# Optimization experiments

Hardware: AMD Instinct MI355X
Metric: run time of the kernel (lower is better)

## Reference

```python
import jax, jax.numpy as jnp
import numpy as np

H, W = 2000, 1000  # T_out buffer: (1, 2000, 1000); conv spatial grid matches
FILL = -9999.0


def _winit(k, o, c):
    return jax.random.normal(k, (o, c), jnp.float32) * (1.0 / np.sqrt(c))


def setup_inputs() -> dict:
    key = jax.random.key(0)
    ks = jax.random.split(key, 6)
    inp = jax.random.normal(ks[0], (1, 9, H, W), dtype=jnp.float32)
    T_out = jnp.zeros((1, H, W), dtype=jnp.float32)
    flat = jnp.arange(H * W, dtype=jnp.int32)
    T_indices = jnp.stack([flat // W, flat % W]).reshape(2, H, W)
    return {
        "input": inp,
        "T_out": T_out,
        "T_indices": T_indices,
        "w1": _winit(ks[1], 18, 9), "b1": jnp.zeros((18,), jnp.float32),
        "w2": _winit(ks[2], 36, 18), "b2": jnp.zeros((36,), jnp.float32),
        "w3": _winit(ks[3], 36, 36), "b3": jnp.zeros((36,), jnp.float32),
        "w4": _winit(ks[4], 1, 36), "b4": jnp.zeros((1,), jnp.float32),
    }


def _conv1x1(x, w, b):
    # 1x1 conv == channel matmul: x (b,c,h,w), w (o,c)
    return jnp.einsum('bchw,oc->bohw', x, w) + b[None, :, None, None]


def reference(input, T_out, T_indices, w1, b1, w2, b2, w3, b3, w4, b4):
    x = jax.nn.relu(_conv1x1(input, w1, b1))
    x = jax.nn.relu(_conv1x1(x, w2, b2))
    x = jax.nn.relu(_conv1x1(x, w3, b3))
    x = _conv1x1(x, w4, b4)  # (1,1,H,W)
    # fill buffer with -9999 then indexed scatter of the fused scores
    T = jnp.full(T_out.shape, FILL, dtype=T_out.dtype)
    T = T.at[:, T_indices[0], T_indices[1]].set(x[0, 0])
    # MaxPool2d([1,1000]) -> max over W; MaxPool2d([2000,1]) -> max over H
    out1 = T.max(axis=2).squeeze()  # (2000,)
    out2 = T.max(axis=1).squeeze()  # (1000,)
    return (out1, out2)
```

## Files before the change

kernel.cpp:

```cpp
#include <hip/hip_runtime.h>

typedef _Float16 f16x8 __attribute__((ext_vector_type(8)));
typedef _Float16 f16x4 __attribute__((ext_vector_type(4)));
typedef __fp16 h16x2 __attribute__((ext_vector_type(2)));
typedef float f32x4 __attribute__((ext_vector_type(4)));

#define HH 2000
#define WW 1000
#define HWSZ (HH * WW)
#define NEG_INF (-3.0e38f)

__device__ __forceinline__ unsigned fenc(float f) {
    unsigned u = __float_as_uint(f);
    return (u & 0x80000000u) ? ~u : (u | 0x80000000u);
}
__device__ __forceinline__ float fdec(unsigned k) {
    unsigned u = (k & 0x80000000u) ? (k & 0x7fffffffu) : ~k;
    return __uint_as_float(u);
}

__global__ void decode_buckets(unsigned* __restrict__ buck, int n) {
    int i = blockIdx.x * blockDim.x + threadIdx.x;
    if (i < n) {
        unsigned k = buck[i];
        ((float*)buck)[i] = fdec(k);
    }
}


__global__ __launch_bounds__(128) void mlp_max_mfma(
    const float* __restrict__ in,
    const float* __restrict__ w1, const float* __restrict__ b1,
    const float* __restrict__ w2, const float* __restrict__ b2,
    const float* __restrict__ w3, const float* __restrict__ b3,
    const float* __restrict__ w4, const float* __restrict__ b4,
    unsigned* __restrict__ rowbuck, unsigned* __restrict__ colbuck) {
    __shared__ _Float16 albuf[2][2 * 1280];
    __shared__ float rowsm[2][16][16];

    const int tx = threadIdx.x;
    const int wv = threadIdx.y;
    const int px = tx & 15;
    const int q = tx >> 4;

    _Float16* s0buf1 = &albuf[wv][0];
    _Float16* s0buf2 = &albuf[wv][640];
    _Float16* s1buf1 = &albuf[wv][1280];
    _Float16* s1buf2 = &albuf[wv][1920];

    if (q == 0) {
        const f16x4 binit = {(_Float16)1.f, (_Float16)0.f, (_Float16)0.f, (_Float16)0.f};
        *(f16x4*)&s0buf2[px * 40 + 36] = binit;
        *(f16x4*)&s1buf2[px * 40 + 36] = binit;
    }

    f16x8 A1[2], A2[3], A3s0[3], A3s1[3];
#pragma unroll
    for (int t = 0; t < 2; ++t) {
        const int m = t * 16 + px;
#pragma unroll
        for (int j = 0; j < 8; ++j) {
            float v = 0.f;
            if (m < 18) {
                if (j == 0) v = w1[m * 9 + q];
                else if (j == 1) v = w1[m * 9 + 4 + q];
                else if (j == 2) {
                    if (q == 0) v = w1[m * 9 + 8];
                    else if (q == 1) v = b1[m];
                }
            }
            A1[t][j] = (_Float16)v;
        }
    }
#pragma unroll
    for (int t = 0; t < 3; ++t) {
        const int m = t * 16 + px;
#pragma unroll
        for (int j = 0; j < 8; ++j) {
            const int k = q * 8 + j;
            float v = 0.f;
            if (m < 36) {
                if (k < 18) v = w2[m * 18 + k];
                else if (k == 18) v = b2[m];
            }
            A2[t][j] = (_Float16)v;
        }
    }
#pragma unroll
    for (int t = 0; t < 3; ++t) {
        const int m = t * 16 + px;
#pragma unroll
        for (int j = 0; j < 8; ++j) {
            const int k = q * 8 + j;
            float v = 0.f;
            if (m < 36 && k < 32) v = w3[m * 36 + k];
            A3s0[t][j] = (_Float16)v;
            float v2 = 0.f;
            const int k2 = 32 + k;
            if (m < 36) {
                if (k2 < 36) v2 = w3[m * 36 + k2];
                else if (k2 == 36) v2 = b3[m];
            }
            A3s1[t][j] = (_Float16)v2;
        }
    }

    h16x2 w4p[3][2];
#pragma unroll
    for (int t = 0; t < 3; ++t)
#pragma unroll
        for (int i = 0; i < 2; ++i) {
            const int c0 = t * 16 + q * 4 + 2 * i;
            const int c1 = c0 + 1;
            w4p[t][i] = __builtin_amdgcn_cvt_pkrtz(c0 < 36 ? w4[c0] : 0.f,
                                                   c1 < 36 ? w4[c1] : 0.f);
        }
    const float b4s = b4[0];

    const int col = blockIdx.x * 32 + wv * 16 + px;
    const int colc = (col < WW) ? col : (WW - 1);
    const bool colok = (col < WW);
    const int rb = blockIdx.y * 16;

    float colmax = NEG_INF;
    const f32x4 zf4 = {0.f, 0.f, 0.f, 0.f};
    const h16x2 z2 = {(__fp16)0.f, (__fp16)0.f};

    union U8 { f16x8 v; h16x2 h[4]; };
    union U4 { f16x4 v; h16x2 h[2]; };

    const int off0 = q * HWSZ + colc;
    const int off1 = (4 + q) * HWSZ + colc;
    const int off2 = 8 * HWSZ + colc;
    const float j2fill = (q == 1) ? 1.f : 0.f;

    float ca[3], cb[3], na[3], nb[3];

    auto LOAD = [&](int r, float (&v0)[3], float (&v1)[3]) {
        const float* rbase = in + (size_t)r * WW;
        v0[0] = rbase[off0]; v1[0] = rbase[off0 + WW];
        v0[1] = rbase[off1]; v1[1] = rbase[off1 + WW];
        float x0 = j2fill, x1 = j2fill;
        if (q == 0) { x0 = rbase[off2]; x1 = rbase[off2 + WW]; }
        v0[2] = x0; v1[2] = x1;
    };

    auto COMPUTE = [&](int it, const float (&v0)[3], const float (&v1)[3]) {
        U8 b0u, b1u;
        b0u.h[0] = __builtin_amdgcn_cvt_pkrtz(v0[0], v0[1]);
        b0u.h[1] = __builtin_amdgcn_cvt_pkrtz(v0[2], 0.f);
        b0u.h[2] = z2; b0u.h[3] = z2;
        b1u.h[0] = __builtin_amdgcn_cvt_pkrtz(v1[0], v1[1]);
        b1u.h[1] = __builtin_amdgcn_cvt_pkrtz(v1[2], 0.f);
        b1u.h[2] = z2; b1u.h[3] = z2;
        const f16x8 bin0 = b0u.v;
        const f16x8 bin1 = b1u.v;

        f32x4 D1a[2], D1b[2];
#pragma unroll
        for (int t = 0; t < 2; ++t) {
            D1a[t] = __builtin_amdgcn_mfma_f32_16x16x32_f16(A1[t], bin0, zf4, 0, 0, 0);
            D1b[t] = __builtin_amdgcn_mfma_f32_16x16x32_f16(A1[t], bin1, zf4, 0, 0, 0);
        }
#pragma unroll
        for (int t = 0; t < 2; ++t) {
            U4 h0, h1;
            h0.h[0] = __builtin_elementwise_max(
                __builtin_amdgcn_cvt_pkrtz(D1a[t][0], D1a[t][1]), z2);
            h0.h[1] = __builtin_elementwise_max(
                __builtin_amdgcn_cvt_pkrtz(D1a[t][2], D1a[t][3]), z2);
            h1.h[0] = __builtin_elementwise_max(
                __builtin_amdgcn_cvt_pkrtz(D1b[t][0], D1b[t][1]), z2);
            h1.h[1] = __builtin_elementwise_max(
                __builtin_amdgcn_cvt_pkrtz(D1b[t][2], D1b[t][3]), z2);
            if (t == 1 && q == 0) {
                h0.v[2] = (_Float16)1.f;
                h1.v[2] = (_Float16)1.f;
            }
            *(f16x4*)&s0buf1[px * 40 + t * 16 + q * 4] = h0.v;
            *(f16x4*)&s1buf1[px * 40 + t * 16 + q * 4] = h1.v;
        }
        const f16x8 B2a = *(const f16x8*)&s0buf1[px * 40 + q * 8];
        const f16x8 B2b = *(const f16x8*)&s1buf1[px * 40 + q * 8];

        f32x4 D2a[3], D2b[3];
#pragma unroll
        for (int t = 0; t < 3; ++t) {
            D2a[t] = __builtin_amdgcn_mfma_f32_16x16x32_f16(A2[t], B2a, zf4, 0, 0, 0);
            D2b[t] = __builtin_amdgcn_mfma_f32_16x16x32_f16(A2[t], B2b, zf4, 0, 0, 0);
        }
#pragma unroll
        for (int t = 0; t < 3; ++t) {
            U4 h0, h1;
            h0.h[0] = __builtin_elementwise_max(
                __builtin_amdgcn_cvt_pkrtz(D2a[t][0], D2a[t][1]), z2);
            h0.h[1] = __builtin_elementwise_max(
                __builtin_amdgcn_cvt_pkrtz(D2a[t][2], D2a[t][3]), z2);
            h1.h[0] = __builtin_elementwise_max(
                __builtin_amdgcn_cvt_pkrtz(D2b[t][0], D2b[t][1]), z2);
            h1.h[1] = __builtin_elementwise_max(
                __builtin_amdgcn_cvt_pkrtz(D2b[t][2], D2b[t][3]), z2);
            if (t < 2) {
                *(f16x4*)&s0buf2[px * 40 + t * 16 + q * 4] = h0.v;
                *(f16x4*)&s1buf2[px * 40 + t * 16 + q * 4] = h1.v;
            } else if (q == 0) {
                *(f16x4*)&s0buf2[px * 40 + 32] = h0.v;
                *(f16x4*)&s1buf2[px * 40 + 32] = h1.v;
            }
        }
        const f16x8 B3a0 = *(const f16x8*)&s0buf2[px * 40 + q * 8];
        const f16x8 B3b0 = *(const f16x8*)&s1buf2[px * 40 + q * 8];
        const f16x8 B3a1 = *(const f16x8*)&s0buf2[px * 40 + 32];
        const f16x8 B3b1 = *(const f16x8*)&s1buf2[px * 40 + 32];

        f32x4 D3a[3], D3b[3];
#pragma unroll
        for (int t = 0; t < 3; ++t) {
            D3a[t] = __builtin_amdgcn_mfma_f32_16x16x32_f16(A3s0[t], B3a0, zf4, 0, 0, 0);
            D3a[t] = __builtin_amdgcn_mfma_f32_16x16x32_f16(A3s1[t], B3a1, D3a[t], 0, 0, 0);
            D3b[t] = __builtin_amdgcn_mfma_f32_16x16x32_f16(A3s0[t], B3b0, zf4, 0, 0, 0);
            D3b[t] = __builtin_amdgcn_mfma_f32_16x16x32_f16(A3s1[t], B3b1, D3b[t], 0, 0, 0);
        }

        float sa0 = 0.f, sa1 = 0.f, sb0 = 0.f, sb1 = 0.f;
#pragma unroll
        for (int t = 0; t < 3; ++t) {
            const h16x2 pa0 = __builtin_elementwise_max(
                __builtin_amdgcn_cvt_pkrtz(D3a[t][0], D3a[t][1]), z2);
            const h16x2 pa1 = __builtin_elementwise_max(
                __builtin_amdgcn_cvt_pkrtz(D3a[t][2], D3a[t][3]), z2);
            const h16x2 pb0 = __builtin_elementwise_max(
                __builtin_amdgcn_cvt_pkrtz(D3b[t][0], D3b[t][1]), z2);
            const h16x2 pb1 = __builtin_elementwise_max(
                __builtin_amdgcn_cvt_pkrtz(D3b[t][2], D3b[t][3]), z2);
            sa0 = __builtin_amdgcn_fdot2(pa0, w4p[t][0], sa0, false);
            sa1 = __builtin_amdgcn_fdot2(pa1, w4p[t][1], sa1, false);
            sb0 = __builtin_amdgcn_fdot2(pb0, w4p[t][0], sb0, false);
            sb1 = __builtin_amdgcn_fdot2(pb1, w4p[t][1], sb1, false);
        }
        float sa = sa0 + sa1;
        float sb = sb0 + sb1;
        sa += __shfl_xor(sa, 16, 64); sb += __shfl_xor(sb, 16, 64);
        sa += __shfl_xor(sa, 32, 64); sb += __shfl_xor(sb, 32, 64);
        sa += b4s; sb += b4s;

        sa = colok ? sa : NEG_INF;
        sb = colok ? sb : NEG_INF;
        colmax = fmaxf(colmax, fmaxf(sa, sb));

        if (q == 0) rowsm[wv][it * 2][px] = sa;
        else if (q == 1) rowsm[wv][it * 2 + 1][px] = sb;
    };

    LOAD(rb, ca, cb);
#pragma unroll 1
    for (int it = 0; it < 8; it += 2) {
        LOAD(rb + (it + 1) * 2, na, nb);
        COMPUTE(it, ca, cb);
        if (it < 6) LOAD(rb + (it + 2) * 2, ca, cb);
        COMPUTE(it + 1, na, nb);
    }

    if (q == 0 && colok) atomicMax(&colbuck[col], fenc(colmax));
    if (tx < 16) {
        const f32x4 v0 = *(const f32x4*)&rowsm[wv][tx][0];
        const f32x4 v1 = *(const f32x4*)&rowsm[wv][tx][4];
        const f32x4 v2 = *(const f32x4*)&rowsm[wv][tx][8];
        const f32x4 v3 = *(const f32x4*)&rowsm[wv][tx][12];
        float m = NEG_INF;
#pragma unroll
        for (int j = 0; j < 4; ++j) {
            m = fmaxf(m, fmaxf(fmaxf(v0[j], v1[j]), fmaxf(v2[j], v3[j])));
        }
        atomicMax(&rowbuck[rb + tx], fenc(m));
    }
}

extern "C" void kernel_launch(void* const* d_in, const int* in_sizes, int n_in,
                              void* d_out, int out_size, void* d_ws, size_t ws_size,
                              hipStream_t stream) {
    const float* in = (const float*)d_in[0];
    const float* w1 = (const float*)d_in[3];
    const float* b1 = (const float*)d_in[4];
    const float* w2 = (const float*)d_in[5];
    const float* b2 = (const float*)d_in[6];
    const float* w3 = (const float*)d_in[7];
    const float* b3 = (const float*)d_in[8];
    const float* w4 = (const float*)d_in[9];
    const float* b4 = (const float*)d_in[10];

    unsigned* buck = (unsigned*)d_out;

    (void)hipMemsetAsync(buck, 0, 3000 * sizeof(unsigned), stream);

    dim3 block(64, 2);
    dim3 grid(32, 125);
    mlp_max_mfma<<<grid, block, 0, stream>>>(in, w1, b1, w2, b2, w3, b3, w4, b4,
                                             buck, buck + 2000);

    decode_buckets<<<(3000 + 255) / 256, 256, 0, stream>>>(buck, 3000);
}
```

Baseline: 182.5 us.

## Chain MFMA layers in registers by permuting weight K-order, dropping LDS staging

Reorders the K dimension of the layer-2 and layer-3 weight fragments so that each lane's MFMA accumulator outputs can be fed directly as the B operand of the next MFMA. This removes the per-iteration LDS writes and reads, and the shared buffers, used to transpose activations between layers. Bias columns are injected through a constant packed register. The cost is a more intricate weight-loading permutation that must exactly match the accumulator layout.

```diff
diff --git a/kernel.cpp b/kernel.cpp
--- a/kernel.cpp
+++ b/kernel.cpp
@@ -35,24 +35,12 @@
     const float* __restrict__ w3, const float* __restrict__ b3,
     const float* __restrict__ w4, const float* __restrict__ b4,
     unsigned* __restrict__ rowbuck, unsigned* __restrict__ colbuck) {
-    __shared__ _Float16 albuf[2][2 * 1280];
     __shared__ float rowsm[2][16][16];
 
     const int tx = threadIdx.x;
     const int wv = threadIdx.y;
     const int px = tx & 15;
     const int q = tx >> 4;
-
-    _Float16* s0buf1 = &albuf[wv][0];
-    _Float16* s0buf2 = &albuf[wv][640];
-    _Float16* s1buf1 = &albuf[wv][1280];
-    _Float16* s1buf2 = &albuf[wv][1920];
-
-    if (q == 0) {
-        const f16x4 binit = {(_Float16)1.f, (_Float16)0.f, (_Float16)0.f, (_Float16)0.f};
-        *(f16x4*)&s0buf2[px * 40 + 36] = binit;
-        *(f16x4*)&s1buf2[px * 40 + 36] = binit;
-    }
 
     f16x8 A1[2], A2[3], A3s0[3], A3s1[3];
 #pragma unroll
@@ -77,11 +65,14 @@
         const int m = t * 16 + px;
 #pragma unroll
         for (int j = 0; j < 8; ++j) {
-            const int k = q * 8 + j;
             float v = 0.f;
             if (m < 36) {
-                if (k < 18) v = w2[m * 18 + k];
-                else if (k == 18) v = b2[m];
+                if (j < 4) v = w2[m * 18 + 4 * q + j];
+                else if (q == 0) {
+                    if (j == 4) v = w2[m * 18 + 16];
+                    else if (j == 5) v = w2[m * 18 + 17];
+                    else if (j == 6) v = b2[m];
+                }
             }
             A2[t][j] = (_Float16)v;
         }
@@ -91,15 +82,16 @@
         const int m = t * 16 + px;
 #pragma unroll
         for (int j = 0; j < 8; ++j) {
-            const int k = q * 8 + j;
             float v = 0.f;
-            if (m < 36 && k < 32) v = w3[m * 36 + k];
+            if (m < 36) {
+                const int ch = (j < 4) ? (4 * q + j) : (16 + 4 * q + (j - 4));
+                v = w3[m * 36 + ch];
+            }
             A3s0[t][j] = (_Float16)v;
             float v2 = 0.f;
-            const int k2 = 32 + k;
-            if (m < 36) {
-                if (k2 < 36) v2 = w3[m * 36 + k2];
-                else if (k2 == 36) v2 = b3[m];
+            if (m < 36 && q == 0) {
+                if (j < 4) v2 = w3[m * 36 + 32 + j];
+                else if (j == 4) v2 = b3[m];
             }
             A3s1[t][j] = (_Float16)v2;
         }
@@ -125,9 +117,9 @@
     float colmax = NEG_INF;
     const f32x4 zf4 = {0.f, 0.f, 0.f, 0.f};
     const h16x2 z2 = {(__fp16)0.f, (__fp16)0.f};
+    const h16x2 cB = (q == 0) ? __builtin_amdgcn_cvt_pkrtz(1.f, 0.f) : z2;
 
     union U8 { f16x8 v; h16x2 h[4]; };
-    union U4 { f16x4 v; h16x2 h[2]; };
 
     const int off0 = q * HWSZ + colc;
     const int off1 = (4 + q) * HWSZ + colc;
@@ -145,6 +137,10 @@
         v0[2] = x0; v1[2] = x1;
     };
 
+    auto maxpk = [&](float x, float y) {
+        return __builtin_elementwise_max(__builtin_amdgcn_cvt_pkrtz(x, y), z2);
+    };
+
     auto COMPUTE = [&](int it, const float (&v0)[3], const float (&v1)[3]) {
         U8 b0u, b1u;
         b0u.h[0] = __builtin_amdgcn_cvt_pkrtz(v0[0], v0[1]);
@@ -153,90 +149,65 @@
         b1u.h[0] = __builtin_amdgcn_cvt_pkrtz(v1[0], v1[1]);
         b1u.h[1] = __builtin_amdgcn_cvt_pkrtz(v1[2], 0.f);
         b1u.h[2] = z2; b1u.h[3] = z2;
-        const f16x8 bin0 = b0u.v;
-        const f16x8 bin1 = b1u.v;
 
         f32x4 D1a[2], D1b[2];
 #pragma unroll
         for (int t = 0; t < 2; ++t) {
-            D1a[t] = __builtin_amdgcn_mfma_f32_16x16x32_f16(A1[t], bin0, zf4, 0, 0, 0);
-            D1b[t] = __builtin_amdgcn_mfma_f32_16x16x32_f16(A1[t], bin1, zf4, 0, 0, 0);
-        }
-#pragma unroll
-        for (int t = 0; t < 2; ++t) {
-            U4 h0, h1;
-            h0.h[0] = __builtin_elementwise_max(
-                __builtin_amdgcn_cvt_pkrtz(D1a[t][0], D1a[t][1]), z2);
-            h0.h[1] = __builtin_elementwise_max(
-                __builtin_amdgcn_cvt_pkrtz(D1a[t][2], D1a[t][3]), z2);
-            h1.h[0] = __builtin_elementwise_max(
-                __builtin_amdgcn_cvt_pkrtz(D1b[t][0], D1b[t][1]), z2);
-            h1.h[1] = __builtin_elementwise_max(
-                __builtin_amdgcn_cvt_pkrtz(D1b[t][2], D1b[t][3]), z2);
-            if (t == 1 && q == 0) {
-                h0.v[2] = (_Float16)1.f;
-                h1.v[2] = (_Float16)1.f;
-            }
-            *(f16x4*)&s0buf1[px * 40 + t * 16 + q * 4] = h0.v;
-            *(f16x4*)&s1buf1[px * 40 + t * 16 + q * 4] = h1.v;
-        }
-        const f16x8 B2a = *(const f16x8*)&s0buf1[px * 40 + q * 8];
-        const f16x8 B2b = *(const f16x8*)&s1buf1[px * 40 + q * 8];
+            D1a[t] = __builtin_amdgcn_mfma_f32_16x16x32_f16(A1[t], b0u.v, zf4, 0, 0, 0);
+            D1b[t] = __builtin_amdgcn_mfma_f32_16x16x32_f16(A1[t], b1u.v, zf4, 0, 0, 0);
+        }
+
+        U8 B2a, B2b;
+        B2a.h[0] = maxpk(D1a[0][0], D1a[0][1]);
+        B2a.h[1] = maxpk(D1a[0][2], D1a[0][3]);
+        B2a.h[2] = maxpk(D1a[1][0], D1a[1][1]);
+        B2a.h[3] = cB;
+        B2b.h[0] = maxpk(D1b[0][0], D1b[0][1]);
+        B2b.h[1] = maxpk(D1b[0][2], D1b[0][3]);
+        B2b.h[2] = maxpk(D1b[1][0], D1b[1][1]);
+        B2b.h[3] = cB;
 
         f32x4 D2a[3], D2b[3];
 #pragma unroll
         for (int t = 0; t < 3; ++t) {
-            D2a[t] = __builtin_amdgcn_mfma_f32_16x16x32_f16(A2[t], B2a, zf4, 0, 0, 0);
-            D2b[t] = __builtin_amdgcn_mfma_f32_16x16x32_f16(A2[t], B2b, zf4, 0, 0, 0);
-        }
+            D2a[t] = __builtin_amdgcn_mfma_f32_16x16x32_f16(A2[t], B2a.v, zf4, 0, 0, 0);
+            D2b[t] = __builtin_amdgcn_mfma_f32_16x16x32_f16(A2[t], B2b.v, zf4, 0, 0, 0);
+        }
+
+        U8 B3a0, B3b0, B3a1, B3b1;
+        B3a0.h[0] = maxpk(D2a[0][0], D2a[0][1]);
+        B3a0.h[1] = maxpk(D2a[0][2], D2a[0][3]);
+        B3a0.h[2] = maxpk(D2a[1][0], D2a[1][1]);
+        B3a0.h[3] = maxpk(D2a[1][2], D2a[1][3]);
+        B3a1.h[0] = maxpk(D2a[2][0], D2a[2][1]);
+        B3a1.h[1] = maxpk(D2a[2][2], D2a[2][3]);
+        B3a1.h[2] = cB;
+        B3a1.h[3] = z2;
+        B3b0.h[0] = maxpk(D2b[0][0], D2b[0][1]);
+        B3b0.h[1] = maxpk(D2b[0][2], D2b[0][3]);
+        B3b0.h[2] = maxpk(D2b[1][0], D2b[1][1]);
+        B3b0.h[3] = maxpk(D2b[1][2], D2b[1][3]);
+        B3b1.h[0] = maxpk(D2b[2][0], D2b[2][1]);
+        B3b1.h[1] = maxpk(D2b[2][2], D2b[2][3]);
+        B3b1.h[2] = cB;
+        B3b1.h[3] = z2;
+
+        f32x4 D3a[3], D3b[3];
 #pragma unroll
         for (int t = 0; t < 3; ++t) {
-            U4 h0, h1;
-            h0.h[0] = __builtin_elementwise_max(
-                __builtin_amdgcn_cvt_pkrtz(D2a[t][0], D2a[t][1]), z2);
-            h0.h[1] = __builtin_elementwise_max(
-                __builtin_amdgcn_cvt_pkrtz(D2a[t][2], D2a[t][3]), z2);
-            h1.h[0] = __builtin_elementwise_max(
-                __builtin_amdgcn_cvt_pkrtz(D2b[t][0], D2b[t][1]), z2);
-            h1.h[1] = __builtin_elementwise_max(
-                __builtin_amdgcn_cvt_pkrtz(D2b[t][2], D2b[t][3]), z2);
-            if (t < 2) {
-                *(f16x4*)&s0buf2[px * 40 + t * 16 + q * 4] = h0.v;
-                *(f16x4*)&s1buf2[px * 40 + t * 16 + q * 4] = h1.v;
-            } else if (q == 0) {
-                *(f16x4*)&s0buf2[px * 40 + 32] = h0.v;
-                *(f16x4*)&s1buf2[px * 40 + 32] = h1.v;
-            }
-        }
-        const f16x8 B3a0 = *(const f16x8*)&s0buf2[px * 40 + q * 8];
-        const f16x8 B3b0 = *(const f16x8*)&s1buf2[px * 40 + q * 8];
-        const f16x8 B3a1 = *(const f16x8*)&s0buf2[px * 40 + 32];
-        const f16x8 B3b1 = *(const f16x8*)&s1buf2[px * 40 + 32];
-
-        f32x4 D3a[3], D3b[3];
+            D3a[t] = __builtin_amdgcn_mfma_f32_16x16x32_f16(A3s0[t], B3a0.v, zf4, 0, 0, 0);
+            D3a[t] = __builtin_amdgcn_mfma_f32_16x16x32_f16(A3s1[t], B3a1.v, D3a[t], 0, 0, 0);
+            D3b[t] = __builtin_amdgcn_mfma_f32_16x16x32_f16(A3s0[t], B3b0.v, zf4, 0, 0, 0);
+            D3b[t] = __builtin_amdgcn_mfma_f32_16x16x32_f16(A3s1[t], B3b1.v, D3b[t], 0, 0, 0);
+        }
+
+        float sa0 = 0.f, sa1 = 0.f, sb0 = 0.f, sb1 = 0.f;
 #pragma unroll
         for (int t = 0; t < 3; ++t) {
-            D3a[t] = __builtin_amdgcn_mfma_f32_16x16x32_f16(A3s0[t], B3a0, zf4, 0, 0, 0);
-            D3a[t] = __builtin_amdgcn_mfma_f32_16x16x32_f16(A3s1[t], B3a1, D3a[t], 0, 0, 0);
-            D3b[t] = __builtin_amdgcn_mfma_f32_16x16x32_f16(A3s0[t], B3b0, zf4, 0, 0, 0);
-            D3b[t] = __builtin_amdgcn_mfma_f32_16x16x32_f16(A3s1[t], B3b1, D3b[t], 0, 0, 0);
-        }
-
-        float sa0 = 0.f, sa1 = 0.f, sb0 = 0.f, sb1 = 0.f;
-#pragma unroll
-        for (int t = 0; t < 3; ++t) {
-            const h16x2 pa0 = __builtin_elementwise_max(
-                __builtin_amdgcn_cvt_pkrtz(D3a[t][0], D3a[t][1]), z2);
-            const h16x2 pa1 = __builtin_elementwise_max(
-                __builtin_amdgcn_cvt_pkrtz(D3a[t][2], D3a[t][3]), z2);
-            const h16x2 pb0 = __builtin_elementwise_max(
-                __builtin_amdgcn_cvt_pkrtz(D3b[t][0], D3b[t][1]), z2);
-            const h16x2 pb1 = __builtin_elementwise_max(
-                __builtin_amdgcn_cvt_pkrtz(D3b[t][2], D3b[t][3]), z2);
-            sa0 = __builtin_amdgcn_fdot2(pa0, w4p[t][0], sa0, false);
-            sa1 = __builtin_amdgcn_fdot2(pa1, w4p[t][1], sa1, false);
-            sb0 = __builtin_amdgcn_fdot2(pb0, w4p[t][0], sb0, false);
-            sb1 = __builtin_amdgcn_fdot2(pb1, w4p[t][1], sb1, false);
+            sa0 = __builtin_amdgcn_fdot2(maxpk(D3a[t][0], D3a[t][1]), w4p[t][0], sa0, false);
+            sa1 = __builtin_amdgcn_fdot2(maxpk(D3a[t][2], D3a[t][3]), w4p[t][1], sa1, false);
+            sb0 = __builtin_amdgcn_fdot2(maxpk(D3b[t][0], D3b[t][1]), w4p[t][0], sb0, false);
+            sb1 = __builtin_amdgcn_fdot2(maxpk(D3b[t][2], D3b[t][3]), w4p[t][1], sb1, false);
         }
         float sa = sa0 + sa1;
         float sb = sb0 + sb1;
```

Result: faster. 175.1 us (-4.1%).
